# Performance work log

Measured on AMD Instinct MI355X. Metric: run time of the kernel, lower is better.

## Reference

```python
import jax, jax.numpy as jnp
import numpy as np

B, S, D, H = 2, 2048, 1024, 16
HD = D // H  # 64


def setup_inputs() -> dict:
    key = jax.random.key(0)
    k1, k2, k3, k4, k5, k6 = jax.random.split(key, 6)
    x = jax.random.normal(k1, (B, S, D), dtype=jnp.float32)
    # binary mask source (1.0 = masked-out position), multiplied by -1e9 inside
    mask = (jax.random.uniform(k2, (B, S, S), dtype=jnp.float32) < 0.1).astype(jnp.float32)
    lim = 1.0 / np.sqrt(D)
    Wqkv = jax.random.uniform(k3, (D, 3 * D), dtype=jnp.float32, minval=-lim, maxval=lim)
    bqkv = jax.random.uniform(k4, (3 * D,), dtype=jnp.float32, minval=-lim, maxval=lim)
    Wo = jax.random.uniform(k5, (D, D), dtype=jnp.float32, minval=-lim, maxval=lim)
    bo = jax.random.uniform(k6, (D,), dtype=jnp.float32, minval=-lim, maxval=lim)
    return {"x": x, "mask": mask, "Wqkv": Wqkv, "bqkv": bqkv, "Wo": Wo, "bo": bo}


def reference(x, mask, Wqkv, bqkv, Wo, bo):
    b, s, d = x.shape
    qkv = x @ Wqkv + bqkv                              # [B,S,3D]
    qkv = qkv.reshape(b, s, 3, H, HD).transpose(2, 0, 3, 1, 4)  # [3,B,H,S,HD]
    q, k, v = qkv[0], qkv[1], qkv[2]
    scale = 1.0 / jnp.sqrt(jnp.float32(HD))
    scores = jnp.einsum('bhqd,bhkd->bhqk', q, k) * scale
    scores = scores + mask[:, None, :, :] * (-1e9)     # broadcast over heads
    attn = jax.nn.softmax(scores, axis=-1)             # [B,H,S,S]
    values = jnp.einsum('bhqk,bhkd->bhqd', attn, v)    # [B,H,S,HD]
    # faithful to source: permute(1,0,2,3) then reshape(B,S,H*HD)
    values = values.transpose(1, 0, 2, 3).reshape(b, s, H * HD)
    return values @ Wo + bo
```

## Files before the change

kernel.cpp:

```cpp
#include <hip/hip_runtime.h>
#include <stdint.h>

#define BB 2
#define SS 2048
#define DD 1024
#define HH 16
#define HD 64
#define BH 32
#define BS 4096

typedef short bf16x8 __attribute__((ext_vector_type(8)));
typedef float f32x4 __attribute__((ext_vector_type(4)));

static __device__ __forceinline__ unsigned short f2bf(float f) {
    union { float f; unsigned int u; } x;
    x.f = f;
    unsigned int u = x.u;
    unsigned int r = u + 0x7FFFu + ((u >> 16) & 1u);
    return (unsigned short)(r >> 16);
}

static __device__ __forceinline__ void gld16(unsigned short* lds, const unsigned short* g) {
    __builtin_amdgcn_global_load_lds(
        (const __attribute__((address_space(1))) unsigned int*)g,
        (__attribute__((address_space(3))) unsigned int*)lds,
        16, 0, 0);
}

__global__ __launch_bounds__(256) void prep(
    const float* __restrict__ x, unsigned short* __restrict__ xb,
    const float* __restrict__ Wqkv, unsigned short* __restrict__ WqkvT,
    const float* __restrict__ Wo, unsigned short* __restrict__ WoT,
    const float* __restrict__ mask, unsigned int* __restrict__ mbitsT) {
    __shared__ float tile[32][33];
    int bid = blockIdx.x;
    int tid = threadIdx.x;
    if (bid < 4096) {
        int i = (bid * 256 + tid) * 4;
        float4 v = *(const float4*)(x + i);
        ushort4 o;
        o.x = f2bf(v.x); o.y = f2bf(v.y); o.z = f2bf(v.z); o.w = f2bf(v.w);
        *(ushort4*)(xb + i) = o;
    } else if (bid < 8192) {
        const float* W;
        unsigned short* WT;
        int N, t;
        if (bid < 7168) { W = Wqkv; WT = WqkvT; N = 3072; t = bid - 4096; }
        else            { W = Wo;   WT = WoT;   N = 1024; t = bid - 7168; }
        const int K = 1024;
        int nx = N >> 5;
        int n0 = (t % nx) * 32, k0 = (t / nx) * 32;
        int tx = tid & 31, ty = tid >> 5;
#pragma unroll
        for (int i = 0; i < 4; i++)
            tile[ty + i * 8][tx] = W[(size_t)(k0 + ty + i * 8) * N + n0 + tx];
        __syncthreads();
#pragma unroll
        for (int i = 0; i < 4; i++)
            WT[(size_t)(n0 + ty + i * 8) * K + k0 + tx] = f2bf(tile[tx][ty + i * 8]);
    } else {
        size_t i = (size_t)(bid - 8192) * 256 + tid;
        float v = mask[i];
        unsigned long long bal = __ballot(v != 0.0f);
        int lane = tid & 63;
        int kw = (int)((i & 2047) >> 5);
        int sq = (int)((i >> 11) & 2047);
        int b = (int)(i >> 22);
        if (lane == 0)
            mbitsT[((size_t)b * 64 + kw) * 2048 + sq] = (unsigned int)bal;
        else if (lane == 32)
            mbitsT[((size_t)b * 64 + kw) * 2048 + sq] = (unsigned int)(bal >> 32);
    }
}

__global__ __launch_bounds__(256) void k_norm_max(
    const unsigned short* __restrict__ k_ws, unsigned int* __restrict__ kmaxsq) {
    int bh = blockIdx.x >> 3, part = blockIdx.x & 7;
    int row = part * 256 + threadIdx.x;
    const unsigned short* rp = k_ws + ((size_t)bh * 2048 + row) * 64;
    float ss = 0.f;
#pragma unroll
    for (int i = 0; i < 64; i += 8) {
        bf16x8 v;
        __builtin_memcpy(&v, rp + i, 16);
#pragma unroll
        for (int j = 0; j < 8; j++) {
            float f = __uint_as_float(((unsigned int)(unsigned short)v[j]) << 16);
            ss += f * f;
        }
    }
#pragma unroll
    for (int d = 1; d < 64; d <<= 1) ss = fmaxf(ss, __shfl_xor(ss, d, 64));
    if ((threadIdx.x & 63) == 0) atomicMax(kmaxsq + bh, __float_as_uint(ss));
}

template <int KDIM>
static __device__ __forceinline__ void mm128_loop(
    const unsigned short* __restrict__ A, const unsigned short* __restrict__ Bt,
    int m0, int n0, unsigned short* ldsA, unsigned short* ldsB, f32x4 acc[4][4]) {
    int tid = threadIdx.x;
    int w = tid >> 6, lane = tid & 63, quad = lane >> 4, l15 = lane & 15;

    int r = tid >> 2, p = tid & 3;
    int c = (p - (r >> 1)) & 3;
    const unsigned short* gA0 = A + (size_t)(m0 + r) * KDIM + c * 8;
    const unsigned short* gA1 = gA0 + (size_t)64 * KDIM;
    const unsigned short* gB0 = Bt + (size_t)(n0 + r) * KDIM + c * 8;
    const unsigned short* gB1 = gB0 + (size_t)64 * KDIM;
    unsigned short* lA0 = ldsA + w * 512;
    unsigned short* lA1 = ldsA + 2048 + w * 512;
    unsigned short* lB0 = ldsB + w * 512;
    unsigned short* lB1 = ldsB + 2048 + w * 512;

    int wm = w >> 1, wn = w & 1;
    int posq = ((quad + (l15 >> 1)) & 3) * 8;
    int aoff = (wm * 64 + l15) * 32 + posq;
    int boff = (wn * 64 + l15) * 32 + posq;

    for (int k0 = 0; k0 < KDIM; k0 += 32) {
        __syncthreads();
        gld16(lA0, gA0 + k0);
        gld16(lA1, gA1 + k0);
        gld16(lB0, gB0 + k0);
        gld16(lB1, gB1 + k0);
        __syncthreads();
        bf16x8 af[4], bfr[4];
#pragma unroll
        for (int i = 0; i < 4; i++) {
            af[i]  = *(const bf16x8*)(ldsA + aoff + i * 512);
            bfr[i] = *(const bf16x8*)(ldsB + boff + i * 512);
        }
#pragma unroll
        for (int i = 0; i < 4; i++)
#pragma unroll
            for (int j = 0; j < 4; j++)
                acc[i][j] = __builtin_amdgcn_mfma_f32_16x16x32_bf16(af[i], bfr[j], acc[i][j], 0, 0, 0);
    }
}

__global__ __launch_bounds__(256) void qkv_gemm(
    const unsigned short* __restrict__ xb,
    const unsigned short* __restrict__ WqkvT,
    const float* __restrict__ bqkv,
    unsigned short* __restrict__ q_ws,
    unsigned short* __restrict__ k_ws,
    unsigned short* __restrict__ vB) {
    __shared__ unsigned short ldsA[4096], ldsB[4096];
    int gx = blockIdx.x;
    int m0 = (gx / 24) * 128, n0 = (gx % 24) * 128;

    f32x4 acc[4][4] = {};
    mm128_loop<1024>(xb, WqkvT, m0, n0, ldsA, ldsB, acc);

    int tid = threadIdx.x;
    int w = tid >> 6, lane = tid & 63, quad = lane >> 4, l15 = lane & 15;
    int wm = w >> 1, wn = w & 1;
    int t = n0 >> 10;
    int ncol0 = n0 + wn * 64;
    int hh = (ncol0 >> 6) & 15;
    int Rb = m0 + wm * 64 + quad * 4;

    if (t == 2) {
        int rowbase = m0 + wm * 64;
        int b = rowbase >> 11;
        int kt = (rowbase >> 6) & 31;
        int bh = b * 16 + hh;
#pragma unroll
        for (int j = 0; j < 4; j++) {
            int hd = j * 16 + l15;
            float bias = bqkv[ncol0 + hd];
#pragma unroll
            for (int i = 0; i < 4; i++) {
                unsigned short* dst = vB +
                    (((((size_t)bh * 32 + kt) * 2 + (i >> 1)) * 4 + quad) * 64 + hd) * 8 + (i & 1) * 4;
                ushort4 pk;
                pk.x = f2bf(acc[i][j][0] + bias);
                pk.y = f2bf(acc[i][j][1] + bias);
                pk.z = f2bf(acc[i][j][2] + bias);
                pk.w = f2bf(acc[i][j][3] + bias);
                *(ushort4*)dst = pk;
            }
        }
    } else {
        unsigned short* dst = (t == 0) ? q_ws : k_ws;
#pragma unroll
        for (int j = 0; j < 4; j++) {
            int hd = j * 16 + l15;
            float bias = bqkv[ncol0 + hd];
#pragma unroll
            for (int i = 0; i < 4; i++) {
                int row = Rb + i * 16;
                int b = row >> 11, s = row & 2047;
                int bh = b * 16 + hh;
#pragma unroll
                for (int rr = 0; rr < 4; rr++)
                    dst[((size_t)(bh * 2048 + s + rr)) * 64 + hd] = f2bf(acc[i][j][rr] + bias);
            }
        }
    }
}

__global__ __launch_bounds__(256) void out_gemm(
    const unsigned short* __restrict__ Amat,
    const unsigned short* __restrict__ WoT,
    const float* __restrict__ bo,
    float* __restrict__ out) {
    __shared__ unsigned short ldsA[4096], ldsB[4096];
    int gx = blockIdx.x;
    int m0 = (gx / 8) * 128, n0 = (gx % 8) * 128;

    f32x4 acc[4][4] = {};
    mm128_loop<1024>(Amat, WoT, m0, n0, ldsA, ldsB, acc);

    int tid = threadIdx.x;
    int w = tid >> 6, lane = tid & 63, quad = lane >> 4, l15 = lane & 15;
    int wm = w >> 1, wn = w & 1;
    int ncol0 = n0 + wn * 64;
    int Rb = m0 + wm * 64 + quad * 4;
#pragma unroll
    for (int j = 0; j < 4; j++) {
        int col = ncol0 + j * 16 + l15;
        float bias = bo[col];
#pragma unroll
        for (int i = 0; i < 4; i++) {
            int row = Rb + i * 16;
#pragma unroll
            for (int rr = 0; rr < 4; rr++)
                out[(size_t)(row + rr) * 1024 + col] = acc[i][j][rr] + bias;
        }
    }
}

__global__ __launch_bounds__(256) void attn(
    const unsigned short* __restrict__ q_ws,
    const unsigned short* __restrict__ k_ws,
    const unsigned short* __restrict__ vB,
    const unsigned int* __restrict__ mbitsT,
    const unsigned int* __restrict__ kmaxsq,
    unsigned short* __restrict__ o_ws) {
    __shared__ unsigned short ldsK[4096];
    __shared__ unsigned short ldsV[4096];

    int tid = threadIdx.x;
    int w = tid >> 6, lane = tid & 63, quad = lane >> 4, l15 = lane & 15;
    int bx = blockIdx.x;
    int bh = bx >> 5, qt = bx & 31;
    int b = bh >> 4, h = bh & 15;

    int q = qt * 64 + w * 16 + l15;
    const unsigned short* qptr = q_ws + ((size_t)(bh * 2048 + q)) * 64 + quad * 8;
    bf16x8 qf0 = *(const bf16x8*)(qptr);
    bf16x8 qf1 = *(const bf16x8*)(qptr + 32);

    float ss = 0.f;
#pragma unroll
    for (int j = 0; j < 8; j++) {
        float a = __uint_as_float(((unsigned int)(unsigned short)qf0[j]) << 16);
        float c = __uint_as_float(((unsigned int)(unsigned short)qf1[j]) << 16);
        ss += a * a + c * c;
    }
    ss += __shfl_xor(ss, 16, 64);
    ss += __shfl_xor(ss, 32, 64);
    const float c2 = 0.125f * 1.44269504089f;
    float Km = sqrtf(__uint_as_float(kmaxsq[bh]));
    float M = sqrtf(ss) * Km * c2 * 1.0002f + 0.03f;
    const float Cs = c2 * 8388608.0f;
    float Ds = (127.0f - M) * 8388608.0f;

    const unsigned int* mb = mbitsT + (size_t)b * 64 * 2048 + q;
    const unsigned short* kbase = k_ws + (size_t)bh * 2048 * 64;
    const unsigned short* vbb = vB + (size_t)bh * 32 * 4096;

    int srow = (lane >> 3);
    int spos = lane & 7;
    unsigned short* dK0 = ldsK + w * 1024 + lane * 8;
    unsigned short* dK1 = dK0 + 512;
    unsigned short* dV0 = ldsV + w * 1024 + lane * 8;
    unsigned short* dV1 = dV0 + 512;
    int r0 = w * 16 + srow;
    int r1 = r0 + 8;
    int g0 = spos ^ (r0 & 7);
    int g1 = spos ^ (r1 & 7);

    f32x4 oacc[4] = {};
    f32x4 lacc = {};
    bf16x8 onesA;
#pragma unroll
    for (int j = 0; j < 8; j++) onesA[j] = (short)0x3F80;

    int sw = (l15 & 7);
    for (int kt = 0; kt < 32; kt++) {
        __syncthreads();
        gld16(dK0, kbase + ((size_t)(kt * 64 + r0)) * 64 + g0 * 8);
        gld16(dK1, kbase + ((size_t)(kt * 64 + r1)) * 64 + g1 * 8);
        {
            const unsigned short* vsrc = vbb + (size_t)kt * 4096 + w * 1024 + lane * 8;
            gld16(dV0, vsrc);
            gld16(dV1, vsrc + 512);
        }
        __syncthreads();

        f32x4 sacc[4];
#pragma unroll
        for (int nt = 0; nt < 4; nt++) {
            const unsigned short* kr = ldsK + (nt * 16 + l15) * 64;
            bf16x8 kf0, kf1;
            __builtin_memcpy(&kf0, kr + (quad ^ sw) * 8, 16);
            __builtin_memcpy(&kf1, kr + ((quad + 4) ^ sw) * 8, 16);
            f32x4 z = {};
            z = __builtin_amdgcn_mfma_f32_16x16x32_bf16(kf0, qf0, z, 0, 0, 0);
            z = __builtin_amdgcn_mfma_f32_16x16x32_bf16(kf1, qf1, z, 0, 0, 0);
            sacc[nt] = z;
        }
        unsigned int w0 = mb[(size_t)(2 * kt) * 2048];
        unsigned int w1 = mb[(size_t)(2 * kt + 1) * 2048];
        unsigned int dw[4][2];
#pragma unroll
        for (int nt = 0; nt < 4; nt++) {
            unsigned int wd = (nt & 2) ? w1 : w0;
            unsigned int u[4];
#pragma unroll
            for (int r = 0; r < 4; r++) {
                float y = __builtin_fmaf(sacc[nt][r], Cs, Ds);
                if ((wd >> ((nt & 1) * 16 + quad * 4 + r)) & 1u) y = 0.f;
                u[r] = (unsigned int)(int)y;
            }
            dw[nt][0] = __builtin_amdgcn_perm(u[1], u[0], 0x07060302u);
            dw[nt][1] = __builtin_amdgcn_perm(u[3], u[2], 0x07060302u);
        }
#pragma unroll
        for (int ks2 = 0; ks2 < 2; ks2++) {
            union { bf16x8 v; unsigned int d[4]; } bfr;
            bfr.d[0] = dw[2 * ks2][0];
            bfr.d[1] = dw[2 * ks2][1];
            bfr.d[2] = dw[2 * ks2 + 1][0];
            bfr.d[3] = dw[2 * ks2 + 1][1];
#pragma unroll
            for (int nb = 0; nb < 4; nb++) {
                bf16x8 vf;
                __builtin_memcpy(&vf, ldsV + ((ks2 * 4 + quad) * 64 + nb * 16 + l15) * 8, 16);
                oacc[nb] = __builtin_amdgcn_mfma_f32_16x16x32_bf16(vf, bfr.v, oacc[nb], 0, 0, 0);
            }
            lacc = __builtin_amdgcn_mfma_f32_16x16x32_bf16(onesA, bfr.v, lacc, 0, 0, 0);
        }
    }

    float linv = 1.0f / lacc[0];
    unsigned short* base = o_ws + ((size_t)((h * 2 + b) * 2048 + q)) * 64;
#pragma unroll
    for (int nb = 0; nb < 4; nb++) {
        ushort4 pk;
        pk.x = f2bf(oacc[nb][0] * linv);
        pk.y = f2bf(oacc[nb][1] * linv);
        pk.z = f2bf(oacc[nb][2] * linv);
        pk.w = f2bf(oacc[nb][3] * linv);
        *(ushort4*)(base + nb * 16 + quad * 4) = pk;
    }
}


extern "C" void kernel_launch(void* const* d_in, const int* in_sizes, int n_in,
                              void* d_out, int out_size, void* d_ws, size_t ws_size,
                              hipStream_t stream) {
    const float* x    = (const float*)d_in[0];
    const float* mask = (const float*)d_in[1];
    const float* Wqkv = (const float*)d_in[2];
    const float* bqkv = (const float*)d_in[3];
    const float* Wo   = (const float*)d_in[4];
    const float* bo   = (const float*)d_in[5];
    float* out = (float*)d_out;

    char* ws = (char*)d_ws;
    unsigned short* xb    = (unsigned short*)(ws);
    unsigned short* WqkvT = (unsigned short*)(ws + ((size_t)8 << 20));
    unsigned short* WoT   = (unsigned short*)(ws + ((size_t)14 << 20));
    unsigned short* q_ws  = (unsigned short*)(ws + ((size_t)16 << 20));
    unsigned short* k_ws  = (unsigned short*)(ws + ((size_t)24 << 20));
    unsigned short* vB    = (unsigned short*)(ws + ((size_t)32 << 20));
    unsigned short* o_ws  = (unsigned short*)(ws + ((size_t)40 << 20));
    unsigned int*   mbits = (unsigned int*)(ws + ((size_t)48 << 20));
    unsigned int*   kmaxsq = (unsigned int*)(ws);

    prep<<<40960, 256, 0, stream>>>(x, xb, Wqkv, WqkvT, Wo, WoT, mask, mbits);
    qkv_gemm<<<32 * 24, 256, 0, stream>>>(xb, WqkvT, bqkv, q_ws, k_ws, vB);
    hipMemsetAsync(kmaxsq, 0, BH * sizeof(unsigned int), stream);
    k_norm_max<<<BH * 8, 256, 0, stream>>>(k_ws, kmaxsq);
    attn<<<1024, 256, 0, stream>>>(q_ws, k_ws, vB, mbits, kmaxsq, o_ws);
    out_gemm<<<32 * 8, 256, 0, stream>>>(o_ws, WoT, bo, out);
}
```

Before: 247.2 us.

## Fuse K-norm into QKV epilogue, double-buffer attention K/V, retile out GEMM

Computes the per-head maximum K row norm inside the QKV GEMM epilogue with shuffles and an atomicMax, which removes the separate k_norm_max kernel and the memset. Mask bit-packing moves from prep into extra blocks of the QKV GEMM launch. The attention kernel now double-buffers its K/V LDS tiles so the next tile's loads overlap compute. The output GEMM uses 128x64 tiles to launch 512 blocks instead of 256. The softmax max-bound margin is widened, and the mask load moves earlier in the loop.

```diff
diff --git a/kernel.cpp b/kernel.cpp
--- a/kernel.cpp
+++ b/kernel.cpp
@@ -31,7 +31,7 @@
     const float* __restrict__ x, unsigned short* __restrict__ xb,
     const float* __restrict__ Wqkv, unsigned short* __restrict__ WqkvT,
     const float* __restrict__ Wo, unsigned short* __restrict__ WoT,
-    const float* __restrict__ mask, unsigned int* __restrict__ mbitsT) {
+    unsigned int* __restrict__ kmaxsq) {
     __shared__ float tile[32][33];
     int bid = blockIdx.x;
     int tid = threadIdx.x;
@@ -59,7 +59,26 @@
         for (int i = 0; i < 4; i++)
             WT[(size_t)(n0 + ty + i * 8) * K + k0 + tx] = f2bf(tile[tx][ty + i * 8]);
     } else {
-        size_t i = (size_t)(bid - 8192) * 256 + tid;
+        if (tid < BH) kmaxsq[tid] = 0u;
+    }
+}
+
+__global__ __launch_bounds__(256) void qkv_gemm(
+    const unsigned short* __restrict__ xb,
+    const unsigned short* __restrict__ WqkvT,
+    const float* __restrict__ bqkv,
+    unsigned short* __restrict__ q_ws,
+    unsigned short* __restrict__ k_ws,
+    unsigned short* __restrict__ vB,
+    const float* __restrict__ mask,
+    unsigned int* __restrict__ mbitsT,
+    unsigned int* __restrict__ kmaxsq) {
+    __shared__ unsigned short ldsA[4096], ldsB[4096];
+    int gx = blockIdx.x;
+    int tid = threadIdx.x;
+
+    if (gx >= 768) {
+        size_t i = (size_t)(gx - 768) * 256 + tid;
         float v = mask[i];
         unsigned long long bal = __ballot(v != 0.0f);
         int lane = tid & 63;
@@ -70,43 +89,18 @@
             mbitsT[((size_t)b * 64 + kw) * 2048 + sq] = (unsigned int)bal;
         else if (lane == 32)
             mbitsT[((size_t)b * 64 + kw) * 2048 + sq] = (unsigned int)(bal >> 32);
-    }
-}
-
-__global__ __launch_bounds__(256) void k_norm_max(
-    const unsigned short* __restrict__ k_ws, unsigned int* __restrict__ kmaxsq) {
-    int bh = blockIdx.x >> 3, part = blockIdx.x & 7;
-    int row = part * 256 + threadIdx.x;
-    const unsigned short* rp = k_ws + ((size_t)bh * 2048 + row) * 64;
-    float ss = 0.f;
-#pragma unroll
-    for (int i = 0; i < 64; i += 8) {
-        bf16x8 v;
-        __builtin_memcpy(&v, rp + i, 16);
-#pragma unroll
-        for (int j = 0; j < 8; j++) {
-            float f = __uint_as_float(((unsigned int)(unsigned short)v[j]) << 16);
-            ss += f * f;
-        }
-    }
-#pragma unroll
-    for (int d = 1; d < 64; d <<= 1) ss = fmaxf(ss, __shfl_xor(ss, d, 64));
-    if ((threadIdx.x & 63) == 0) atomicMax(kmaxsq + bh, __float_as_uint(ss));
-}
-
-template <int KDIM>
-static __device__ __forceinline__ void mm128_loop(
-    const unsigned short* __restrict__ A, const unsigned short* __restrict__ Bt,
-    int m0, int n0, unsigned short* ldsA, unsigned short* ldsB, f32x4 acc[4][4]) {
-    int tid = threadIdx.x;
+        return;
+    }
+
+    int m0 = (gx / 24) * 128, n0 = (gx % 24) * 128;
     int w = tid >> 6, lane = tid & 63, quad = lane >> 4, l15 = lane & 15;
 
     int r = tid >> 2, p = tid & 3;
     int c = (p - (r >> 1)) & 3;
-    const unsigned short* gA0 = A + (size_t)(m0 + r) * KDIM + c * 8;
-    const unsigned short* gA1 = gA0 + (size_t)64 * KDIM;
-    const unsigned short* gB0 = Bt + (size_t)(n0 + r) * KDIM + c * 8;
-    const unsigned short* gB1 = gB0 + (size_t)64 * KDIM;
+    const unsigned short* gA0 = xb + (size_t)(m0 + r) * 1024 + c * 8;
+    const unsigned short* gA1 = gA0 + (size_t)64 * 1024;
+    const unsigned short* gB0 = WqkvT + (size_t)(n0 + r) * 1024 + c * 8;
+    const unsigned short* gB1 = gB0 + (size_t)64 * 1024;
     unsigned short* lA0 = ldsA + w * 512;
     unsigned short* lA1 = ldsA + 2048 + w * 512;
     unsigned short* lB0 = ldsB + w * 512;
@@ -117,7 +111,8 @@
     int aoff = (wm * 64 + l15) * 32 + posq;
     int boff = (wn * 64 + l15) * 32 + posq;
 
-    for (int k0 = 0; k0 < KDIM; k0 += 32) {
+    f32x4 acc[4][4] = {};
+    for (int k0 = 0; k0 < 1024; k0 += 32) {
         __syncthreads();
         gld16(lA0, gA0 + k0);
         gld16(lA1, gA1 + k0);
@@ -136,25 +131,7 @@
             for (int j = 0; j < 4; j++)
                 acc[i][j] = __builtin_amdgcn_mfma_f32_16x16x32_bf16(af[i], bfr[j], acc[i][j], 0, 0, 0);
     }
-}
-
-__global__ __launch_bounds__(256) void qkv_gemm(
-    const unsigned short* __restrict__ xb,
-    const unsigned short* __restrict__ WqkvT,
-    const float* __restrict__ bqkv,
-    unsigned short* __restrict__ q_ws,
-    unsigned short* __restrict__ k_ws,
-    unsigned short* __restrict__ vB) {
-    __shared__ unsigned short ldsA[4096], ldsB[4096];
-    int gx = blockIdx.x;
-    int m0 = (gx / 24) * 128, n0 = (gx % 24) * 128;
-
-    f32x4 acc[4][4] = {};
-    mm128_loop<1024>(xb, WqkvT, m0, n0, ldsA, ldsB, acc);
-
-    int tid = threadIdx.x;
-    int w = tid >> 6, lane = tid & 63, quad = lane >> 4, l15 = lane & 15;
-    int wm = w >> 1, wn = w & 1;
+
     int t = n0 >> 10;
     int ncol0 = n0 + wn * 64;
     int hh = (ncol0 >> 6) & 15;
@@ -183,6 +160,11 @@
         }
     } else {
         unsigned short* dst = (t == 0) ? q_ws : k_ws;
+        float rs[4][4];
+#pragma unroll
+        for (int i = 0; i < 4; i++)
+#pragma unroll
+            for (int rr = 0; rr < 4; rr++) rs[i][rr] = 0.f;
 #pragma unroll
         for (int j = 0; j < 4; j++) {
             int hd = j * 16 + l15;
@@ -193,8 +175,30 @@
                 int b = row >> 11, s = row & 2047;
                 int bh = b * 16 + hh;
 #pragma unroll
-                for (int rr = 0; rr < 4; rr++)
-                    dst[((size_t)(bh * 2048 + s + rr)) * 64 + hd] = f2bf(acc[i][j][rr] + bias);
+                for (int rr = 0; rr < 4; rr++) {
+                    float v = acc[i][j][rr] + bias;
+                    dst[((size_t)(bh * 2048 + s + rr)) * 64 + hd] = f2bf(v);
+                    rs[i][rr] += v * v;
+                }
+            }
+        }
+        if (t == 1) {
+            float kmax = 0.f;
+#pragma unroll
+            for (int i = 0; i < 4; i++)
+#pragma unroll
+                for (int rr = 0; rr < 4; rr++) {
+                    float rsum = rs[i][rr];
+                    rsum += __shfl_xor(rsum, 1, 16);
+                    rsum += __shfl_xor(rsum, 2, 16);
+                    rsum += __shfl_xor(rsum, 4, 16);
+                    rsum += __shfl_xor(rsum, 8, 16);
+                    kmax = fmaxf(kmax, rsum);
+                }
+            if (l15 == 0) {
+                int rowbase = m0 + wm * 64;
+                int bh = (rowbase >> 11) * 16 + hh;
+                atomicMax(kmaxsq + bh, __float_as_uint(kmax));
             }
         }
     }
@@ -205,20 +209,48 @@
     const unsigned short* __restrict__ WoT,
     const float* __restrict__ bo,
     float* __restrict__ out) {
-    __shared__ unsigned short ldsA[4096], ldsB[4096];
+    __shared__ unsigned short ldsA[4096], ldsB[2048];
     int gx = blockIdx.x;
-    int m0 = (gx / 8) * 128, n0 = (gx % 8) * 128;
-
-    f32x4 acc[4][4] = {};
-    mm128_loop<1024>(Amat, WoT, m0, n0, ldsA, ldsB, acc);
-
+    int m0 = (gx / 16) * 128, n0 = (gx % 16) * 64;
     int tid = threadIdx.x;
     int w = tid >> 6, lane = tid & 63, quad = lane >> 4, l15 = lane & 15;
+
+    int r = tid >> 2, p = tid & 3;
+    int c = (p - (r >> 1)) & 3;
+    const unsigned short* gA0 = Amat + (size_t)(m0 + r) * 1024 + c * 8;
+    const unsigned short* gA1 = gA0 + (size_t)64 * 1024;
+    const unsigned short* gB0 = WoT + (size_t)(n0 + r) * 1024 + c * 8;
+    unsigned short* lA0 = ldsA + w * 512;
+    unsigned short* lA1 = ldsA + 2048 + w * 512;
+    unsigned short* lB0 = ldsB + w * 512;
+
     int wm = w >> 1, wn = w & 1;
-    int ncol0 = n0 + wn * 64;
+    int posq = ((quad + (l15 >> 1)) & 3) * 8;
+    int aoff = (wm * 64 + l15) * 32 + posq;
+    int boff = (wn * 32 + l15) * 32 + posq;
+
+    f32x4 acc[4][2] = {};
+    for (int k0 = 0; k0 < 1024; k0 += 32) {
+        __syncthreads();
+        gld16(lA0, gA0 + k0);
+        gld16(lA1, gA1 + k0);
+        gld16(lB0, gB0 + k0);
+        __syncthreads();
+        bf16x8 af[4], bfr[2];
+#pragma unroll
+        for (int i = 0; i < 4; i++) af[i] = *(const bf16x8*)(ldsA + aoff + i * 512);
+#pragma unroll
+        for (int j = 0; j < 2; j++) bfr[j] = *(const bf16x8*)(ldsB + boff + j * 512);
+#pragma unroll
+        for (int i = 0; i < 4; i++)
+#pragma unroll
+            for (int j = 0; j < 2; j++)
+                acc[i][j] = __builtin_amdgcn_mfma_f32_16x16x32_bf16(af[i], bfr[j], acc[i][j], 0, 0, 0);
+    }
+    int ncol0 = n0 + wn * 32;
     int Rb = m0 + wm * 64 + quad * 4;
 #pragma unroll
-    for (int j = 0; j < 4; j++) {
+    for (int j = 0; j < 2; j++) {
         int col = ncol0 + j * 16 + l15;
         float bias = bo[col];
 #pragma unroll
@@ -238,8 +270,8 @@
     const unsigned int* __restrict__ mbitsT,
     const unsigned int* __restrict__ kmaxsq,
     unsigned short* __restrict__ o_ws) {
-    __shared__ unsigned short ldsK[4096];
-    __shared__ unsigned short ldsV[4096];
+    __shared__ unsigned short ldsK[2][4096];
+    __shared__ unsigned short ldsV[2][4096];
 
     int tid = threadIdx.x;
     int w = tid >> 6, lane = tid & 63, quad = lane >> 4, l15 = lane & 15;
@@ -263,7 +295,7 @@
     ss += __shfl_xor(ss, 32, 64);
     const float c2 = 0.125f * 1.44269504089f;
     float Km = sqrtf(__uint_as_float(kmaxsq[bh]));
-    float M = sqrtf(ss) * Km * c2 * 1.0002f + 0.03f;
+    float M = sqrtf(ss) * Km * c2 * 1.01f + 0.05f;
     const float Cs = c2 * 8388608.0f;
     float Ds = (127.0f - M) * 8388608.0f;
 
@@ -273,14 +305,12 @@
 
     int srow = (lane >> 3);
     int spos = lane & 7;
-    unsigned short* dK0 = ldsK + w * 1024 + lane * 8;
-    unsigned short* dK1 = dK0 + 512;
-    unsigned short* dV0 = ldsV + w * 1024 + lane * 8;
-    unsigned short* dV1 = dV0 + 512;
     int r0 = w * 16 + srow;
     int r1 = r0 + 8;
     int g0 = spos ^ (r0 & 7);
     int g1 = spos ^ (r1 & 7);
+    unsigned short* dK0 = &ldsK[0][0] + w * 1024 + lane * 8;
+    unsigned short* dV0 = &ldsV[0][0] + w * 1024 + lane * 8;
 
     f32x4 oacc[4] = {};
     f32x4 lacc = {};
@@ -289,21 +319,37 @@
     for (int j = 0; j < 8; j++) onesA[j] = (short)0x3F80;
 
     int sw = (l15 & 7);
+    int q4 = quad * 4;
+
+    {
+        gld16(dK0, kbase + ((size_t)r0) * 64 + g0 * 8);
+        gld16(dK0 + 512, kbase + ((size_t)r1) * 64 + g1 * 8);
+        const unsigned short* vsrc = vbb + w * 1024 + lane * 8;
+        gld16(dV0, vsrc);
+        gld16(dV0 + 512, vsrc + 512);
+    }
+
     for (int kt = 0; kt < 32; kt++) {
-        __syncthreads();
-        gld16(dK0, kbase + ((size_t)(kt * 64 + r0)) * 64 + g0 * 8);
-        gld16(dK1, kbase + ((size_t)(kt * 64 + r1)) * 64 + g1 * 8);
-        {
-            const unsigned short* vsrc = vbb + (size_t)kt * 4096 + w * 1024 + lane * 8;
-            gld16(dV0, vsrc);
-            gld16(dV1, vsrc + 512);
-        }
-        __syncthreads();
-
+        int cur = kt & 1;
+        __syncthreads();
+        if (kt < 31) {
+            int nb2 = (cur ^ 1) * 4096;
+            size_t kb = (size_t)((kt + 1) * 64);
+            gld16(dK0 + nb2, kbase + (kb + r0) * 64 + g0 * 8);
+            gld16(dK0 + nb2 + 512, kbase + (kb + r1) * 64 + g1 * 8);
+            const unsigned short* vsrc = vbb + (size_t)(kt + 1) * 4096 + w * 1024 + lane * 8;
+            gld16(dV0 + nb2, vsrc);
+            gld16(dV0 + nb2 + 512, vsrc + 512);
+        }
+        unsigned int w0 = mb[(size_t)(2 * kt) * 2048];
+        unsigned int w1 = mb[(size_t)(2 * kt + 1) * 2048];
+
+        const unsigned short* Kc = &ldsK[cur][0];
+        const unsigned short* Vc = &ldsV[cur][0];
         f32x4 sacc[4];
 #pragma unroll
         for (int nt = 0; nt < 4; nt++) {
-            const unsigned short* kr = ldsK + (nt * 16 + l15) * 64;
+            const unsigned short* kr = Kc + (nt * 16 + l15) * 64;
             bf16x8 kf0, kf1;
             __builtin_memcpy(&kf0, kr + (quad ^ sw) * 8, 16);
             __builtin_memcpy(&kf1, kr + ((quad + 4) ^ sw) * 8, 16);
@@ -312,18 +358,18 @@
             z = __builtin_amdgcn_mfma_f32_16x16x32_bf16(kf1, qf1, z, 0, 0, 0);
             sacc[nt] = z;
         }
-        unsigned int w0 = mb[(size_t)(2 * kt) * 2048];
-        unsigned int w1 = mb[(size_t)(2 * kt + 1) * 2048];
+        unsigned int s0 = w0 >> q4;
+        unsigned int s1 = w1 >> q4;
         unsigned int dw[4][2];
 #pragma unroll
         for (int nt = 0; nt < 4; nt++) {
-            unsigned int wd = (nt & 2) ? w1 : w0;
+            unsigned int sel = (nt & 2) ? s1 : s0;
             unsigned int u[4];
 #pragma unroll
-            for (int r = 0; r < 4; r++) {
-                float y = __builtin_fmaf(sacc[nt][r], Cs, Ds);
-                if ((wd >> ((nt & 1) * 16 + quad * 4 + r)) & 1u) y = 0.f;
-                u[r] = (unsigned int)(int)y;
+            for (int rr = 0; rr < 4; rr++) {
+                float y = __builtin_fmaf(sacc[nt][rr], Cs, Ds);
+                if ((sel >> ((nt & 1) * 16 + rr)) & 1u) y = 0.f;
+                u[rr] = (unsigned int)(int)y;
             }
             dw[nt][0] = __builtin_amdgcn_perm(u[1], u[0], 0x07060302u);
             dw[nt][1] = __builtin_amdgcn_perm(u[3], u[2], 0x07060302u);
@@ -338,7 +384,7 @@
 #pragma unroll
             for (int nb = 0; nb < 4; nb++) {
                 bf16x8 vf;
-                __builtin_memcpy(&vf, ldsV + ((ks2 * 4 + quad) * 64 + nb * 16 + l15) * 8, 16);
+                __builtin_memcpy(&vf, Vc + ((ks2 * 4 + quad) * 64 + nb * 16 + l15) * 8, 16);
                 oacc[nb] = __builtin_amdgcn_mfma_f32_16x16x32_bf16(vf, bfr.v, oacc[nb], 0, 0, 0);
             }
             lacc = __builtin_amdgcn_mfma_f32_16x16x32_bf16(onesA, bfr.v, lacc, 0, 0, 0);
@@ -379,12 +425,11 @@
     unsigned short* vB    = (unsigned short*)(ws + ((size_t)32 << 20));
     unsigned short* o_ws  = (unsigned short*)(ws + ((size_t)40 << 20));
     unsigned int*   mbits = (unsigned int*)(ws + ((size_t)48 << 20));
-    unsigned int*   kmaxsq = (unsigned int*)(ws);
-
-    prep<<<40960, 256, 0, stream>>>(x, xb, Wqkv, WqkvT, Wo, WoT, mask, mbits);
-    qkv_gemm<<<32 * 24, 256, 0, stream>>>(xb, WqkvT, bqkv, q_ws, k_ws, vB);
-    hipMemsetAsync(kmaxsq, 0, BH * sizeof(unsigned int), stream);
-    k_norm_max<<<BH * 8, 256, 0, stream>>>(k_ws, kmaxsq);
+    unsigned int*   kmaxsq = (unsigned int*)(ws + ((size_t)49 << 20));
+
+    prep<<<8193, 256, 0, stream>>>(x, xb, Wqkv, WqkvT, Wo, WoT, kmaxsq);
+    qkv_gemm<<<768 + 32768, 256, 0, stream>>>(xb, WqkvT, bqkv, q_ws, k_ws, vB,
+                                              mask, mbits, kmaxsq);
     attn<<<1024, 256, 0, stream>>>(q_ws, k_ws, vB, mbits, kmaxsq, o_ws);
-    out_gemm<<<32 * 8, 256, 0, stream>>>(o_ws, WoT, bo, out);
-}
+    out_gemm<<<512, 256, 0, stream>>>(o_ws, WoT, bo, out);
+}
```

Result: slower. 287.7 us (+16.4%).
